# Performance work log

Hardware: AMD Instinct MI355X
Metric: run time of the kernel (lower is better)

The kernel has to match this reference:

```python
import jax, jax.numpy as jnp
import numpy as np
from jax import lax

DIM = 384
HEADS = 8
HEAD_DIM = DIM // HEADS
EPS = 1e-06


def setup_inputs() -> dict:
    key = jax.random.key(0)
    ks = jax.random.split(key, 16)
    B, N, C = 8, 4096, DIM
    s = 0.02
    inp = {
        "x": jax.random.normal(ks[0], (B, N, C), jnp.float32),
        "wq": jax.random.normal(ks[1], (C, C), jnp.float32) * s,
        "bq": jnp.zeros((C,), jnp.float32),
        "wk": jax.random.normal(ks[2], (C, C), jnp.float32) * s,
        "bk": jnp.zeros((C,), jnp.float32),
        "wv": jax.random.normal(ks[3], (C, C), jnp.float32) * s,
        "bv": jnp.zeros((C,), jnp.float32),
        "wg": jax.random.normal(ks[4], (C, C), jnp.float32) * s,
        "bg": jnp.zeros((C,), jnp.float32),
        "wo": jax.random.normal(ks[5], (C, C), jnp.float32) * s,
        "bo": jnp.zeros((C,), jnp.float32),
        "temperature": jnp.ones((HEADS, 1, 1), jnp.float32),
        "dw_w": jax.random.normal(ks[6], (C, 1, 3, 3), jnp.float32) * s,  # depthwise 3x3
        "dw_b": jnp.zeros((C,), jnp.float32),
        "pw_w": jax.random.normal(ks[7], (C, C), jnp.float32) * s,        # pointwise 1x1
        "pw_b": jnp.zeros((C,), jnp.float32),
    }
    return inp


def _phi(x):
    # exp(x - max) over last dim, numerically stable
    return jnp.exp(x - jnp.max(x, axis=-1, keepdims=True))


def _token_mixer(x, dw_w, dw_b, pw_w, pw_b):
    B, N, C = x.shape
    H = W = int(np.sqrt(N))
    feat = x.transpose(0, 2, 1).reshape(B, C, H, W)
    feat = lax.conv_general_dilated(
        feat, dw_w, window_strides=(1, 1), padding=((1, 1), (1, 1)),
        feature_group_count=C, dimension_numbers=("NCHW", "OIHW", "NCHW"))
    feat = feat + dw_b[None, :, None, None]
    feat = jnp.einsum("bchw,oc->bohw", feat, pw_w) + pw_b[None, :, None, None]
    return feat.reshape(B, C, N).transpose(0, 2, 1)


def reference(x, wq, bq, wk, bk, wv, bv, wg, bg, wo, bo, temperature,
              dw_w, dw_b, pw_w, pw_b):
    B, N, C = x.shape
    residual = x
    x = x + _token_mixer(x, dw_w, dw_b, pw_w, pw_b)

    def heads(y):  # [B,N,C] -> [B,H,N,d]
        return y.reshape(B, N, HEADS, HEAD_DIM).transpose(0, 2, 1, 3)

    q = heads(jnp.einsum("bnc,oc->bno", x, wq) + bq)
    k = heads(jnp.einsum("bnc,oc->bno", x, wk) + bk)
    v = heads(jnp.einsum("bnc,oc->bno", x, wv) + bv)
    g = heads(jnp.einsum("bnc,oc->bno", x, wg) + bg)

    q = _phi(q * temperature[None])       # temperature: [H,1,1] broadcasts over [B,H,N,d]
    k = _phi(k)
    v = v * jax.nn.sigmoid(g)

    kv = jnp.einsum("bhnd,bhne->bhde", k, v)     # [B,H,d,d]
    k_sum = jnp.sum(k, axis=2)                   # [B,H,d]
    num = jnp.einsum("bhnd,bhde->bhne", q, kv)   # [B,H,N,d]
    den = jnp.einsum("bhnd,bhd->bhn", q, k_sum)[..., None] + EPS
    out = num / den

    out = out.transpose(0, 2, 1, 3).reshape(B, N, C)
    out = jnp.einsum("bnc,oc->bno", out, wo) + bo
    return out + 0.0 * residual
```

## Files before the change

### kernel.cpp

```cpp
#include <hip/hip_runtime.h>
#include <math.h>

#define EPSF 1e-6f

typedef __attribute__((ext_vector_type(8))) short bf16x8;
typedef __attribute__((ext_vector_type(4))) float f32x4;
typedef unsigned short u16;
typedef unsigned int u32;

#define MFMA16(a,b,c) __builtin_amdgcn_mfma_f32_16x16x32_bf16((a),(b),(c),0,0,0)

__device__ __forceinline__ float bf2f(u16 u){
  union { u32 i; float f; } x; x.i = ((u32)u)<<16; return x.f;
}
__device__ __forceinline__ u16 f2bf(float f){
  u32 x = __builtin_bit_cast(u32, f);
  u32 r = (x + 0x7fffu + ((x >> 16) & 1u)) >> 16;
  return (u16)r;
}
__device__ __forceinline__ void gll16(const void* g, void* l){
  __builtin_amdgcn_global_load_lds(
      (const __attribute__((address_space(1))) u32*)g,
      (__attribute__((address_space(3))) u32*)l, 16, 0, 0);
}

__global__ __launch_bounds__(256) void k0_prep(
    const float* __restrict__ wq, const float* __restrict__ bq,
    const float* __restrict__ wk, const float* __restrict__ bk,
    const float* __restrict__ wv, const float* __restrict__ bv,
    const float* __restrict__ wg, const float* __restrict__ bg,
    const float* __restrict__ pw_w, const float* __restrict__ wo,
    u16* __restrict__ wpack, u16* __restrict__ pwb, u16* __restrict__ wob,
    float* __restrict__ bpack, float* __restrict__ kvacc, float* __restrict__ ksumacc)
{
  int idx = blockIdx.x*256 + threadIdx.x;
  const int NW = 1536*384;
  if (idx < NW) {
    int r = idx / 384, c = idx - r*384;
    int h = r / 192, s = (r % 192)/48, d = r % 48;
    const float* w = (s==0)?wq:(s==1)?wk:(s==2)?wv:wg;
    wpack[idx] = f2bf(w[(h*48+d)*384 + c]);
    if (c==0){
      const float* b = (s==0)?bq:(s==1)?bk:(s==2)?bv:bg;
      bpack[r] = b[h*48+d];
    }
  } else if (idx < NW + 147456) {
    pwb[idx - NW] = f2bf(pw_w[idx - NW]);
  } else if (idx < NW + 2*147456) {
    wob[idx - NW - 147456] = f2bf(wo[idx - NW - 147456]);
  } else if (idx < NW + 2*147456 + 147456) {
    kvacc[idx - NW - 2*147456] = 0.f;
  } else if (idx < NW + 2*147456 + 147456 + 3072) {
    ksumacc[idx - NW - 2*147456 - 147456] = 0.f;
  }
}

__global__ __launch_bounds__(256) void k1_dw(
    const float* __restrict__ x, const float* __restrict__ dw_w,
    const float* __restrict__ dw_b, u16* __restrict__ t)
{
  int idx = blockIdx.x*256 + threadIdx.x;
  int c4 = idx % 96; int rest = idx / 96;
  int jg = rest & 15; rest >>= 4;
  int i = rest & 63; int b = rest >> 6;
  int c0 = c4*4, j0 = jg*4;
  float wf[36];
  {
    const float4* wp = (const float4*)(dw_w + c0*9);
    #pragma unroll
    for (int k=0;k<9;k++){
      float4 v = wp[k];
      wf[4*k] = v.x; wf[4*k+1] = v.y; wf[4*k+2] = v.z; wf[4*k+3] = v.w;
    }
  }
  float4 bias = *(const float4*)(dw_b + c0);
  float acc[4][4];
  #pragma unroll
  for (int tk=0;tk<4;tk++){
    acc[tk][0]=bias.x; acc[tk][1]=bias.y; acc[tk][2]=bias.z; acc[tk][3]=bias.w;
  }
  const float* xb = x + ((size_t)b<<12)*384;
  #pragma unroll
  for (int di=-1; di<=1; ++di){
    int ii = i+di; if ((unsigned)ii >= 64u) continue;
    #pragma unroll
    for (int dj=-1; dj<=4; ++dj){
      int jj = j0+dj; if ((unsigned)jj >= 64u) continue;
      float4 xv = *(const float4*)(xb + (size_t)((ii<<6)+jj)*384 + c0);
      #pragma unroll
      for (int tk=0;tk<4;tk++){
        const int dd = dj - tk;
        if (dd < -1 || dd > 1) continue;
        const int tap = (di+1)*3 + (dd+1);
        acc[tk][0] = fmaf(xv.x, wf[0*9+tap], acc[tk][0]);
        acc[tk][1] = fmaf(xv.y, wf[1*9+tap], acc[tk][1]);
        acc[tk][2] = fmaf(xv.z, wf[2*9+tap], acc[tk][2]);
        acc[tk][3] = fmaf(xv.w, wf[3*9+tap], acc[tk][3]);
      }
    }
  }
  int mbase = (b<<12) + (i<<6) + j0;
  #pragma unroll
  for (int tk=0;tk<4;tk++){
    ushort4 o; o.x=f2bf(acc[tk][0]); o.y=f2bf(acc[tk][1]);
    o.z=f2bf(acc[tk][2]); o.w=f2bf(acc[tk][3]);
    *(ushort4*)(t + (size_t)(mbase+tk)*384 + c0) = o;
  }
}

__global__ __launch_bounds__(256) void k2_gemm_pw(
    const u16* __restrict__ t, const u16* __restrict__ pwb,
    const float* __restrict__ x, const float* __restrict__ pw_b,
    u16* __restrict__ xm)
{
  __shared__ __align__(16) u16 As[128*64];
  __shared__ __align__(16) u16 Bs[128*64];
  const int m0 = blockIdx.x * 128;
  const int n0 = blockIdx.y * 128;
  const int tid = threadIdx.x, w = tid>>6, l = tid&63;
  const f32x4 zf = {0.f,0.f,0.f,0.f};
  f32x4 acc[4][4];
  #pragma unroll
  for (int i=0;i<4;i++)
    #pragma unroll
    for (int j=0;j<4;j++) acc[i][j] = zf;

  for (int k0=0; k0<384; k0+=64) {
    #pragma unroll
    for (int i=0;i<4;i++){
      int ch = w*4+i;
      int row = ch*8 + (l>>3);
      gll16((const char*)t   + ((size_t)(m0+row)*384 + k0)*2 + (l&7)*16, (char*)As + ch*1024);
      gll16((const char*)pwb + ((size_t)(n0+row)*384 + k0)*2 + (l&7)*16, (char*)Bs + ch*1024);
    }
    __syncthreads();
    const int wr = (w>>1)*64, wc = (w&1)*64;
    #pragma unroll
    for (int kk=0; kk<64; kk+=32){
      bf16x8 a[4], bb[4];
      #pragma unroll
      for (int i=0;i<4;i++) a[i]  = *(const bf16x8*)&As[(wr + i*16 + (l&15))*64 + kk + (l>>4)*8];
      #pragma unroll
      for (int j=0;j<4;j++) bb[j] = *(const bf16x8*)&Bs[(wc + j*16 + (l&15))*64 + kk + (l>>4)*8];
      #pragma unroll
      for (int i=0;i<4;i++)
        #pragma unroll
        for (int j=0;j<4;j++)
          acc[i][j] = MFMA16(a[i], bb[j], acc[i][j]);
    }
    __syncthreads();
  }
  const int wr=(w>>1)*64, wc=(w&1)*64;
  #pragma unroll
  for (int j=0;j<4;j++){
    int n = n0 + wc + j*16 + (l&15);
    float bias = pw_b[n];
    #pragma unroll
    for (int i=0;i<4;i++)
      #pragma unroll
      for (int r=0;r<4;r++){
        int m = m0 + wr + i*16 + (l>>4)*4 + r;
        float v = acc[i][j][r] + x[(size_t)m*384 + n] + bias;
        xm[(size_t)m*384 + n] = f2bf(v);
      }
  }
}

__global__ __launch_bounds__(256) void k3_gemm_qkvg(
    const u16* __restrict__ xm, const u16* __restrict__ wpack,
    const float* __restrict__ bpack, const float* __restrict__ temperature,
    u16* __restrict__ qh, float* __restrict__ kvacc, float* __restrict__ ksumacc)
{
  __shared__ __align__(16) u16 smem[20480];
  u16* As = smem;
  u16* Bs = smem + 8192;
  const int m0 = blockIdx.x * 128;
  const int h  = blockIdx.y;
  const int tid = threadIdx.x, w = tid>>6, l = tid&63;
  const int lc = l & 15, hi = l >> 4;
  const f32x4 zf = {0.f,0.f,0.f,0.f};
  f32x4 acc[2][12];
  #pragma unroll
  for (int i=0;i<2;i++)
    #pragma unroll
    for (int j=0;j<12;j++) acc[i][j] = zf;

  for (int k0=0; k0<384; k0+=64){
    #pragma unroll
    for (int i=0;i<4;i++){
      int ch = w*4+i, row = ch*8 + (l>>3);
      gll16((const char*)xm + ((size_t)(m0+row)*384 + k0)*2 + (l&7)*16, (char*)As + ch*1024);
    }
    #pragma unroll
    for (int i=0;i<6;i++){
      int ch = w*6+i, row = ch*8 + (l>>3);
      gll16((const char*)wpack + ((size_t)(h*192+row)*384 + k0)*2 + (l&7)*16, (char*)Bs + ch*1024);
    }
    __syncthreads();
    const int rbase = w*32;
    #pragma unroll
    for (int kk=0; kk<64; kk+=32){
      bf16x8 a0 = *(const bf16x8*)&As[(rbase +      lc)*64 + kk + hi*8];
      bf16x8 a1 = *(const bf16x8*)&As[(rbase + 16 + lc)*64 + kk + hi*8];
      #pragma unroll
      for (int j=0;j<12;j++){
        bf16x8 bb = *(const bf16x8*)&Bs[(j*16 + lc)*64 + kk + hi*8];
        acc[0][j] = MFMA16(a0, bb, acc[0][j]);
        acc[1][j] = MFMA16(a1, bb, acc[1][j]);
      }
    }
    __syncthreads();
  }

  const float tq = temperature[h];
  const int b = m0 >> 12;
  const size_t bh = (size_t)b*8 + h;
  const int bb0 = h*192;
  float biasq[3], biask[3], biasv[3], biasg[3];
  #pragma unroll
  for (int j=0;j<3;j++){
    biasq[j] = bpack[bb0       + j*16 + lc];
    biask[j] = bpack[bb0 + 48  + j*16 + lc];
    biasv[j] = bpack[bb0 + 96  + j*16 + lc];
    biasg[j] = bpack[bb0 + 144 + j*16 + lc];
  }
  u16* kT = smem;
  u16* vT = smem + 6528;
  float ksp[3] = {0.f, 0.f, 0.f};

  #pragma unroll
  for (int i=0;i<2;i++){
    ushort4 kst[3], vst[3];
    #pragma unroll
    for (int r=0;r<4;r++){
      int m = m0 + w*32 + i*16 + hi*4 + r;
      int n = m & 4095;
      size_t rowq = (bh*4096 + n)*64;
      float q0=(acc[i][0][r]+biasq[0])*tq;
      float q1=(acc[i][1][r]+biasq[1])*tq;
      float q2=(acc[i][2][r]+biasq[2])*tq;
      float mx = fmaxf(q0,fmaxf(q1,q2));
      mx = fmaxf(mx, __shfl_xor(mx,1,64));
      mx = fmaxf(mx, __shfl_xor(mx,2,64));
      mx = fmaxf(mx, __shfl_xor(mx,4,64));
      mx = fmaxf(mx, __shfl_xor(mx,8,64));
      qh[rowq +      lc] = f2bf(expf(q0-mx));
      qh[rowq + 16 + lc] = f2bf(expf(q1-mx));
      qh[rowq + 32 + lc] = f2bf(expf(q2-mx));
      qh[rowq + 48 + lc] = 0;
      float s0=acc[i][3][r]+biask[0];
      float s1=acc[i][4][r]+biask[1];
      float s2=acc[i][5][r]+biask[2];
      float mk = fmaxf(s0,fmaxf(s1,s2));
      mk = fmaxf(mk, __shfl_xor(mk,1,64));
      mk = fmaxf(mk, __shfl_xor(mk,2,64));
      mk = fmaxf(mk, __shfl_xor(mk,4,64));
      mk = fmaxf(mk, __shfl_xor(mk,8,64));
      float k0e = expf(s0-mk), k1e = expf(s1-mk), k2e = expf(s2-mk);
      ksp[0] += k0e; ksp[1] += k1e; ksp[2] += k2e;
      u16 kq0=f2bf(k0e), kq1=f2bf(k1e), kq2=f2bf(k2e);
      u16 vq[3];
      #pragma unroll
      for (int j=0;j<3;j++){
        float vv = acc[i][6+j][r] + biasv[j];
        float gg = acc[i][9+j][r] + biasg[j];
        float sg = 1.f/(1.f + expf(-gg));
        vq[j] = f2bf(vv*sg);
      }
      if (r==0){ kst[0].x=kq0; kst[1].x=kq1; kst[2].x=kq2; vst[0].x=vq[0]; vst[1].x=vq[1]; vst[2].x=vq[2]; }
      if (r==1){ kst[0].y=kq0; kst[1].y=kq1; kst[2].y=kq2; vst[0].y=vq[0]; vst[1].y=vq[1]; vst[2].y=vq[2]; }
      if (r==2){ kst[0].z=kq0; kst[1].z=kq1; kst[2].z=kq2; vst[0].z=vq[0]; vst[1].z=vq[1]; vst[2].z=vq[2]; }
      if (r==3){ kst[0].w=kq0; kst[1].w=kq1; kst[2].w=kq2; vst[0].w=vq[0]; vst[1].w=vq[1]; vst[2].w=vq[2]; }
    }
    int mb = w*32 + i*16 + hi*4;
    #pragma unroll
    for (int j=0;j<3;j++){
      *(ushort4*)&kT[(j*16+lc)*136 + mb] = kst[j];
      *(ushort4*)&vT[(j*16+lc)*136 + mb] = vst[j];
    }
  }
  __syncthreads();

  bf16x8 af[3], bfv[3];
  #pragma unroll
  for (int da=0;da<3;da++) af[da]  = *(const bf16x8*)&kT[(da*16+lc)*136 + w*32 + hi*8];
  #pragma unroll
  for (int eb=0;eb<3;eb++) bfv[eb] = *(const bf16x8*)&vT[(eb*16+lc)*136 + w*32 + hi*8];
  f32x4 a2[3][3];
  #pragma unroll
  for (int da=0;da<3;da++)
    #pragma unroll
    for (int eb=0;eb<3;eb++)
      a2[da][eb] = MFMA16(af[da], bfv[eb], zf);
  __syncthreads();
  float* pb = (float*)smem + w*2304;
  #pragma unroll
  for (int da=0;da<3;da++)
    #pragma unroll
    for (int eb=0;eb<3;eb++)
      #pragma unroll
      for (int rr=0;rr<4;rr++)
        pb[(da*16 + hi*4 + rr)*48 + eb*16 + lc] = a2[da][eb][rr];
  __syncthreads();
  float* p0 = (float*)smem;
  for (int u=tid; u<2304; u+=256){
    float s = p0[u] + p0[2304+u] + p0[4608+u] + p0[6912+u];
    atomicAdd(kvacc + bh*2304 + u, s);
  }
  #pragma unroll
  for (int j=0;j<3;j++){
    ksp[j] += __shfl_xor(ksp[j],16,64);
    ksp[j] += __shfl_xor(ksp[j],32,64);
  }
  if (hi==0){
    atomicAdd(ksumacc + bh*48 +      lc, ksp[0]);
    atomicAdd(ksumacc + bh*48 + 16 + lc, ksp[1]);
    atomicAdd(ksumacc + bh*48 + 32 + lc, ksp[2]);
  }
}

__global__ __launch_bounds__(256) void k5_red(
    const float* __restrict__ kvacc, const float* __restrict__ ksumacc,
    u16* __restrict__ kvp)
{
  int bh = blockIdx.x, tid = threadIdx.x;
  for (int u=tid; u<4096; u+=256){
    int e = u >> 6, d = u & 63;
    float v = 0.f;
    if (e < 48 && d < 48)       v = kvacc[(size_t)bh*2304 + d*48 + e];
    else if (e == 48 && d < 48) v = ksumacc[bh*48 + d];
    kvp[((size_t)bh*64 + e)*64 + d] = f2bf(v);
  }
}

__global__ __launch_bounds__(256) void k6_num(
    const u16* __restrict__ qh, const u16* __restrict__ kvp, u16* __restrict__ ah)
{
  __shared__ __align__(16) u16 As[256*64];
  __shared__ __align__(16) u16 Bs[64*64];
  const int bh = blockIdx.x >> 4, nc = blockIdx.x & 15;
  const int tid = threadIdx.x, w = tid>>6, l = tid&63;
  const f32x4 zf = {0.f,0.f,0.f,0.f};
  const uint4* ga = (const uint4*)(qh + ((size_t)bh*4096 + nc*256)*64);
  #pragma unroll
  for (int it=0; it<8; ++it) ((uint4*)As)[it*256+tid] = ga[it*256+tid];
  const uint4* gb = (const uint4*)(kvp + (size_t)bh*4096);
  #pragma unroll
  for (int it=0; it<2; ++it) ((uint4*)Bs)[it*256+tid] = gb[it*256+tid];
  __syncthreads();
  f32x4 acc[4][4];
  #pragma unroll
  for (int i=0;i<4;i++)
    #pragma unroll
    for (int j=0;j<4;j++) acc[i][j] = zf;
  const int rbase = w*64;
  #pragma unroll
  for (int kk=0; kk<64; kk+=32){
    bf16x8 a[4], bb[4];
    #pragma unroll
    for (int i=0;i<4;i++) a[i]  = *(const bf16x8*)&As[(rbase + i*16 + (l&15))*64 + kk + (l>>4)*8];
    #pragma unroll
    for (int j=0;j<4;j++) bb[j] = *(const bf16x8*)&Bs[(j*16 + (l&15))*64 + kk + (l>>4)*8];
    #pragma unroll
    for (int i=0;i<4;i++)
      #pragma unroll
      for (int j=0;j<4;j++)
        acc[i][j] = MFMA16(a[i], bb[j], acc[i][j]);
  }
  const int b = bh >> 3, h = bh & 7;
  #pragma unroll
  for (int i=0;i<4;i++){
    #pragma unroll
    for (int r=0;r<4;r++){
      float den = __shfl(acc[i][3][r], l & 48, 64) + EPSF;
      float rd = 1.f/den;
      int n = nc*256 + rbase + i*16 + (l>>4)*4 + r;
      size_t ob = ((size_t)b*4096 + n)*384 + h*48;
      ah[ob +      (l&15)] = f2bf(acc[i][0][r]*rd);
      ah[ob + 16 + (l&15)] = f2bf(acc[i][1][r]*rd);
      ah[ob + 32 + (l&15)] = f2bf(acc[i][2][r]*rd);
    }
  }
}

__global__ __launch_bounds__(256) void k7_gemm_out(
    const u16* __restrict__ ah, const u16* __restrict__ wob,
    const float* __restrict__ bo, float* __restrict__ out)
{
  __shared__ __align__(16) u16 As[128*64];
  __shared__ __align__(16) u16 Bs[128*64];
  const int m0 = blockIdx.x * 128;
  const int n0 = blockIdx.y * 128;
  const int tid = threadIdx.x, w = tid>>6, l = tid&63;
  const f32x4 zf = {0.f,0.f,0.f,0.f};
  f32x4 acc[4][4];
  #pragma unroll
  for (int i=0;i<4;i++)
    #pragma unroll
    for (int j=0;j<4;j++) acc[i][j] = zf;

  for (int k0=0; k0<384; k0+=64) {
    #pragma unroll
    for (int i=0;i<4;i++){
      int ch = w*4+i;
      int row = ch*8 + (l>>3);
      gll16((const char*)ah  + ((size_t)(m0+row)*384 + k0)*2 + (l&7)*16, (char*)As + ch*1024);
      gll16((const char*)wob + ((size_t)(n0+row)*384 + k0)*2 + (l&7)*16, (char*)Bs + ch*1024);
    }
    __syncthreads();
    const int wr = (w>>1)*64, wc = (w&1)*64;
    #pragma unroll
    for (int kk=0; kk<64; kk+=32){
      bf16x8 a[4], bb[4];
      #pragma unroll
      for (int i=0;i<4;i++) a[i]  = *(const bf16x8*)&As[(wr + i*16 + (l&15))*64 + kk + (l>>4)*8];
      #pragma unroll
      for (int j=0;j<4;j++) bb[j] = *(const bf16x8*)&Bs[(wc + j*16 + (l&15))*64 + kk + (l>>4)*8];
      #pragma unroll
      for (int i=0;i<4;i++)
        #pragma unroll
        for (int j=0;j<4;j++)
          acc[i][j] = MFMA16(a[i], bb[j], acc[i][j]);
    }
    __syncthreads();
  }
  const int wr=(w>>1)*64, wc=(w&1)*64;
  #pragma unroll
  for (int j=0;j<4;j++){
    int n = n0 + wc + j*16 + (l&15);
    float bias = bo[n];
    #pragma unroll
    for (int i=0;i<4;i++)
      #pragma unroll
      for (int r=0;r<4;r++){
        int m = m0 + wr + i*16 + (l>>4)*4 + r;
        out[(size_t)m*384 + n] = acc[i][j][r] + bias;
      }
  }
}

extern "C" void kernel_launch(void* const* d_in, const int* in_sizes, int n_in,
                              void* d_out, int out_size, void* d_ws, size_t ws_size,
                              hipStream_t stream)
{
  const float* x    = (const float*)d_in[0];
  const float* wq   = (const float*)d_in[1];
  const float* bq   = (const float*)d_in[2];
  const float* wk   = (const float*)d_in[3];
  const float* bk   = (const float*)d_in[4];
  const float* wv   = (const float*)d_in[5];
  const float* bv   = (const float*)d_in[6];
  const float* wg   = (const float*)d_in[7];
  const float* bg   = (const float*)d_in[8];
  const float* wo   = (const float*)d_in[9];
  const float* bo   = (const float*)d_in[10];
  const float* temp = (const float*)d_in[11];
  const float* dw_w = (const float*)d_in[12];
  const float* dw_b = (const float*)d_in[13];
  const float* pw_w = (const float*)d_in[14];
  const float* pw_b = (const float*)d_in[15];
  float* out = (float*)d_out;
  char* ws = (char*)d_ws;

  u16*   t       = (u16*)(ws + 0);
  u16*   xm      = (u16*)(ws + 25165824);
  u16*   qh      = (u16*)(ws + 50331648);
  u16*   wpack   = (u16*)(ws + 83886080);
  u16*   pwb     = (u16*)(ws + 85065728);
  u16*   wob     = (u16*)(ws + 85360640);
  float* bpack   = (float*)(ws + 85655552);
  float* kvacc   = (float*)(ws + 85661696);
  float* ksumacc = (float*)(ws + 86251520);
  u16*   kvp     = (u16*)(ws + 86263808);

  k0_prep<<<4044, 256, 0, stream>>>(wq,bq,wk,bk,wv,bv,wg,bg,pw_w,wo,
                                    wpack,pwb,wob,bpack,kvacc,ksumacc);
  k1_dw<<<3072, 256, 0, stream>>>(x, dw_w, dw_b, t);
  k2_gemm_pw<<<dim3(256,3), 256, 0, stream>>>(t, pwb, x, pw_b, xm);
  k3_gemm_qkvg<<<dim3(256,8), 256, 0, stream>>>(xm, wpack, bpack, temp, qh, kvacc, ksumacc);
  k5_red<<<64, 256, 0, stream>>>(kvacc, ksumacc, kvp);
  k6_num<<<1024, 256, 0, stream>>>(qh, kvp, t );
  k7_gemm_out<<<dim3(256,3), 256, 0, stream>>>(t, wob, bo, out);
}
```

Before: 207.2 us.

## Use k-chunk-major LDS layout to avoid bank conflicts and compact q storage

Reorganizes the shared-memory tiles in all GEMM kernels from row-major (64 bf16 per row) to a chunk-major layout where each 8-element k-chunk is contiguous across rows. This is meant to remove LDS bank conflicts on the 16-byte MFMA operand reads. The exp(q) tile is now staged in LDS and written to global memory in a matching chunked layout with 48 instead of 64 columns, which drops the zero padding from the q buffer and cuts its global traffic. The kv buffer layout is changed to match, and the consumer kernel zero-fills the padding chunks in LDS itself. The cost is more complex indexing, an extra LDS staging pass in k3, and a global load pattern where each lane now fetches a different row per 16-byte load.

```diff
diff --git a/kernel.cpp b/kernel.cpp
--- a/kernel.cpp
+++ b/kernel.cpp
@@ -118,6 +118,7 @@
   const int m0 = blockIdx.x * 128;
   const int n0 = blockIdx.y * 128;
   const int tid = threadIdx.x, w = tid>>6, l = tid&63;
+  const int lc = l & 15, hi = l >> 4;
   const f32x4 zf = {0.f,0.f,0.f,0.f};
   f32x4 acc[4][4];
   #pragma unroll
@@ -127,21 +128,22 @@
 
   for (int k0=0; k0<384; k0+=64) {
     #pragma unroll
-    for (int i=0;i<4;i++){
-      int ch = w*4+i;
-      int row = ch*8 + (l>>3);
-      gll16((const char*)t   + ((size_t)(m0+row)*384 + k0)*2 + (l&7)*16, (char*)As + ch*1024);
-      gll16((const char*)pwb + ((size_t)(n0+row)*384 + k0)*2 + (l&7)*16, (char*)Bs + ch*1024);
+    for (int c=0;c<4;c++){
+      int chunk = 2*c + (w>>1);
+      int row = (w&1)*64 + l;
+      gll16((const char*)t   + ((size_t)(m0+row)*384 + k0 + chunk*8)*2, (char*)As + (c*256+w*64)*16);
+      gll16((const char*)pwb + ((size_t)(n0+row)*384 + k0 + chunk*8)*2, (char*)Bs + (c*256+w*64)*16);
     }
     __syncthreads();
     const int wr = (w>>1)*64, wc = (w&1)*64;
     #pragma unroll
     for (int kk=0; kk<64; kk+=32){
+      const int ca = (kk>>3) + hi;
       bf16x8 a[4], bb[4];
       #pragma unroll
-      for (int i=0;i<4;i++) a[i]  = *(const bf16x8*)&As[(wr + i*16 + (l&15))*64 + kk + (l>>4)*8];
-      #pragma unroll
-      for (int j=0;j<4;j++) bb[j] = *(const bf16x8*)&Bs[(wc + j*16 + (l&15))*64 + kk + (l>>4)*8];
+      for (int i=0;i<4;i++) a[i]  = *(const bf16x8*)&As[(ca*128 + wr + i*16 + lc)*8];
+      #pragma unroll
+      for (int j=0;j<4;j++) bb[j] = *(const bf16x8*)&Bs[(ca*128 + wc + j*16 + lc)*8];
       #pragma unroll
       for (int i=0;i<4;i++)
         #pragma unroll
@@ -153,13 +155,13 @@
   const int wr=(w>>1)*64, wc=(w&1)*64;
   #pragma unroll
   for (int j=0;j<4;j++){
-    int n = n0 + wc + j*16 + (l&15);
+    int n = n0 + wc + j*16 + lc;
     float bias = pw_b[n];
     #pragma unroll
     for (int i=0;i<4;i++)
       #pragma unroll
       for (int r=0;r<4;r++){
-        int m = m0 + wr + i*16 + (l>>4)*4 + r;
+        int m = m0 + wr + i*16 + hi*4 + r;
         float v = acc[i][j][r] + x[(size_t)m*384 + n] + bias;
         xm[(size_t)m*384 + n] = f2bf(v);
       }
@@ -187,24 +189,28 @@
 
   for (int k0=0; k0<384; k0+=64){
     #pragma unroll
-    for (int i=0;i<4;i++){
-      int ch = w*4+i, row = ch*8 + (l>>3);
-      gll16((const char*)xm + ((size_t)(m0+row)*384 + k0)*2 + (l&7)*16, (char*)As + ch*1024);
-    }
-    #pragma unroll
-    for (int i=0;i<6;i++){
-      int ch = w*6+i, row = ch*8 + (l>>3);
-      gll16((const char*)wpack + ((size_t)(h*192+row)*384 + k0)*2 + (l&7)*16, (char*)Bs + ch*1024);
+    for (int c=0;c<4;c++){
+      int chunk = 2*c + (w>>1);
+      int row = (w&1)*64 + l;
+      gll16((const char*)xm + ((size_t)(m0+row)*384 + k0 + chunk*8)*2, (char*)As + (c*256+w*64)*16);
+    }
+    #pragma unroll
+    for (int c=0;c<6;c++){
+      int q = c*4 + w;
+      int chunk = q/3;
+      int row = (q - chunk*3)*64 + l;
+      gll16((const char*)wpack + ((size_t)(h*192+row)*384 + k0 + chunk*8)*2, (char*)Bs + q*1024);
     }
     __syncthreads();
     const int rbase = w*32;
     #pragma unroll
     for (int kk=0; kk<64; kk+=32){
-      bf16x8 a0 = *(const bf16x8*)&As[(rbase +      lc)*64 + kk + hi*8];
-      bf16x8 a1 = *(const bf16x8*)&As[(rbase + 16 + lc)*64 + kk + hi*8];
+      const int ca = (kk>>3) + hi;
+      bf16x8 a0 = *(const bf16x8*)&As[(ca*128 + rbase +      lc)*8];
+      bf16x8 a1 = *(const bf16x8*)&As[(ca*128 + rbase + 16 + lc)*8];
       #pragma unroll
       for (int j=0;j<12;j++){
-        bf16x8 bb = *(const bf16x8*)&Bs[(j*16 + lc)*64 + kk + hi*8];
+        bf16x8 bb = *(const bf16x8*)&Bs[(ca*192 + j*16 + lc)*8];
         acc[0][j] = MFMA16(a0, bb, acc[0][j]);
         acc[1][j] = MFMA16(a1, bb, acc[1][j]);
       }
@@ -224,8 +230,9 @@
     biasv[j] = bpack[bb0 + 96  + j*16 + lc];
     biasg[j] = bpack[bb0 + 144 + j*16 + lc];
   }
-  u16* kT = smem;
-  u16* vT = smem + 6528;
+  u16* kT  = smem;
+  u16* vT  = smem + 6528;
+  u16* qls = smem + 13056;
   float ksp[3] = {0.f, 0.f, 0.f};
 
   #pragma unroll
@@ -233,9 +240,7 @@
     ushort4 kst[3], vst[3];
     #pragma unroll
     for (int r=0;r<4;r++){
-      int m = m0 + w*32 + i*16 + hi*4 + r;
-      int n = m & 4095;
-      size_t rowq = (bh*4096 + n)*64;
+      int row = w*32 + i*16 + hi*4 + r;
       float q0=(acc[i][0][r]+biasq[0])*tq;
       float q1=(acc[i][1][r]+biasq[1])*tq;
       float q2=(acc[i][2][r]+biasq[2])*tq;
@@ -244,10 +249,10 @@
       mx = fmaxf(mx, __shfl_xor(mx,2,64));
       mx = fmaxf(mx, __shfl_xor(mx,4,64));
       mx = fmaxf(mx, __shfl_xor(mx,8,64));
-      qh[rowq +      lc] = f2bf(expf(q0-mx));
-      qh[rowq + 16 + lc] = f2bf(expf(q1-mx));
-      qh[rowq + 32 + lc] = f2bf(expf(q2-mx));
-      qh[rowq + 48 + lc] = 0;
+      int ro8 = row*8 + (lc&7);
+      qls[((lc>>3)  )*1024 + ro8] = f2bf(expf(q0-mx));
+      qls[((lc>>3)+2)*1024 + ro8] = f2bf(expf(q1-mx));
+      qls[((lc>>3)+4)*1024 + ro8] = f2bf(expf(q2-mx));
       float s0=acc[i][3][r]+biask[0];
       float s1=acc[i][4][r]+biask[1];
       float s2=acc[i][5][r]+biask[2];
@@ -281,6 +286,18 @@
   }
   __syncthreads();
 
+  {
+    const int tile = (m0 & 4095) >> 8;
+    const int half = (m0 >> 7) & 1;
+    size_t gqb = ((size_t)bh*4096 + tile*256)*48;
+    #pragma unroll
+    for (int it=0; it<3; ++it){
+      int s = it*256 + tid;
+      int g = (s>>7)*256 + half*128 + (s&127);
+      *(uint4*)(qh + gqb + (size_t)g*8) = *(const uint4*)&qls[s*8];
+    }
+  }
+
   bf16x8 af[3], bfv[3];
   #pragma unroll
   for (int da=0;da<3;da++) af[da]  = *(const bf16x8*)&kT[(da*16+lc)*136 + w*32 + hi*8];
@@ -329,7 +346,7 @@
     float v = 0.f;
     if (e < 48 && d < 48)       v = kvacc[(size_t)bh*2304 + d*48 + e];
     else if (e == 48 && d < 48) v = ksumacc[bh*48 + d];
-    kvp[((size_t)bh*64 + e)*64 + d] = f2bf(v);
+    kvp[(size_t)bh*4096 + (d>>3)*512 + e*8 + (d&7)] = f2bf(v);
   }
 }
 
@@ -340,10 +357,14 @@
   __shared__ __align__(16) u16 Bs[64*64];
   const int bh = blockIdx.x >> 4, nc = blockIdx.x & 15;
   const int tid = threadIdx.x, w = tid>>6, l = tid&63;
+  const int lc = l & 15, hi = l >> 4;
   const f32x4 zf = {0.f,0.f,0.f,0.f};
-  const uint4* ga = (const uint4*)(qh + ((size_t)bh*4096 + nc*256)*64);
-  #pragma unroll
-  for (int it=0; it<8; ++it) ((uint4*)As)[it*256+tid] = ga[it*256+tid];
+  const uint4* ga = (const uint4*)(qh + ((size_t)bh*4096 + nc*256)*48);
+  #pragma unroll
+  for (int it=0; it<6; ++it) ((uint4*)As)[it*256+tid] = ga[it*256+tid];
+  uint4 z4 = {0,0,0,0};
+  *(uint4*)&As[(1536+tid)*8] = z4;
+  *(uint4*)&As[(1792+tid)*8] = z4;
   const uint4* gb = (const uint4*)(kvp + (size_t)bh*4096);
   #pragma unroll
   for (int it=0; it<2; ++it) ((uint4*)Bs)[it*256+tid] = gb[it*256+tid];
@@ -356,11 +377,12 @@
   const int rbase = w*64;
   #pragma unroll
   for (int kk=0; kk<64; kk+=32){
+    const int ca = (kk>>3) + hi;
     bf16x8 a[4], bb[4];
     #pragma unroll
-    for (int i=0;i<4;i++) a[i]  = *(const bf16x8*)&As[(rbase + i*16 + (l&15))*64 + kk + (l>>4)*8];
-    #pragma unroll
-    for (int j=0;j<4;j++) bb[j] = *(const bf16x8*)&Bs[(j*16 + (l&15))*64 + kk + (l>>4)*8];
+    for (int i=0;i<4;i++) a[i]  = *(const bf16x8*)&As[(ca*256 + rbase + i*16 + lc)*8];
+    #pragma unroll
+    for (int j=0;j<4;j++) bb[j] = *(const bf16x8*)&Bs[(ca*64 + j*16 + lc)*8];
     #pragma unroll
     for (int i=0;i<4;i++)
       #pragma unroll
@@ -374,11 +396,11 @@
     for (int r=0;r<4;r++){
       float den = __shfl(acc[i][3][r], l & 48, 64) + EPSF;
       float rd = 1.f/den;
-      int n = nc*256 + rbase + i*16 + (l>>4)*4 + r;
+      int n = nc*256 + rbase + i*16 + hi*4 + r;
       size_t ob = ((size_t)b*4096 + n)*384 + h*48;
-      ah[ob +      (l&15)] = f2bf(acc[i][0][r]*rd);
-      ah[ob + 16 + (l&15)] = f2bf(acc[i][1][r]*rd);
-      ah[ob + 32 + (l&15)] = f2bf(acc[i][2][r]*rd);
+      ah[ob +      lc] = f2bf(acc[i][0][r]*rd);
+      ah[ob + 16 + lc] = f2bf(acc[i][1][r]*rd);
+      ah[ob + 32 + lc] = f2bf(acc[i][2][r]*rd);
     }
   }
 }
@@ -392,6 +414,7 @@
   const int m0 = blockIdx.x * 128;
   const int n0 = blockIdx.y * 128;
   const int tid = threadIdx.x, w = tid>>6, l = tid&63;
+  const int lc = l & 15, hi = l >> 4;
   const f32x4 zf = {0.f,0.f,0.f,0.f};
   f32x4 acc[4][4];
   #pragma unroll
@@ -401,21 +424,22 @@
 
   for (int k0=0; k0<384; k0+=64) {
     #pragma unroll
-    for (int i=0;i<4;i++){
-      int ch = w*4+i;
-      int row = ch*8 + (l>>3);
-      gll16((const char*)ah  + ((size_t)(m0+row)*384 + k0)*2 + (l&7)*16, (char*)As + ch*1024);
-      gll16((const char*)wob + ((size_t)(n0+row)*384 + k0)*2 + (l&7)*16, (char*)Bs + ch*1024);
+    for (int c=0;c<4;c++){
+      int chunk = 2*c + (w>>1);
+      int row = (w&1)*64 + l;
+      gll16((const char*)ah  + ((size_t)(m0+row)*384 + k0 + chunk*8)*2, (char*)As + (c*256+w*64)*16);
+      gll16((const char*)wob + ((size_t)(n0+row)*384 + k0 + chunk*8)*2, (char*)Bs + (c*256+w*64)*16);
     }
     __syncthreads();
     const int wr = (w>>1)*64, wc = (w&1)*64;
     #pragma unroll
     for (int kk=0; kk<64; kk+=32){
+      const int ca = (kk>>3) + hi;
       bf16x8 a[4], bb[4];
       #pragma unroll
-      for (int i=0;i<4;i++) a[i]  = *(const bf16x8*)&As[(wr + i*16 + (l&15))*64 + kk + (l>>4)*8];
-      #pragma unroll
-      for (int j=0;j<4;j++) bb[j] = *(const bf16x8*)&Bs[(wc + j*16 + (l&15))*64 + kk + (l>>4)*8];
+      for (int i=0;i<4;i++) a[i]  = *(const bf16x8*)&As[(ca*128 + wr + i*16 + lc)*8];
+      #pragma unroll
+      for (int j=0;j<4;j++) bb[j] = *(const bf16x8*)&Bs[(ca*128 + wc + j*16 + lc)*8];
       #pragma unroll
       for (int i=0;i<4;i++)
         #pragma unroll
@@ -427,13 +451,13 @@
   const int wr=(w>>1)*64, wc=(w&1)*64;
   #pragma unroll
   for (int j=0;j<4;j++){
-    int n = n0 + wc + j*16 + (l&15);
+    int n = n0 + wc + j*16 + lc;
     float bias = bo[n];
     #pragma unroll
     for (int i=0;i<4;i++)
       #pragma unroll
       for (int r=0;r<4;r++){
-        int m = m0 + wr + i*16 + (l>>4)*4 + r;
+        int m = m0 + wr + i*16 + hi*4 + r;
         out[(size_t)m*384 + n] = acc[i][j][r] + bias;
       }
   }
```

Result: slower. 230.4 us (+11.2%).

## Restructure QKVG GEMM into 1024-thread blocks with double-buffered swizzled LDS

Applied to the files above, without the earlier changes.

The QKVG projection kernel now uses 1024-thread blocks, each covering 256 rows. The K loop uses double-buffered LDS stages with XOR-swizzled chunk placement, so the next global-to-LDS load is issued while the current tile feeds the MFMAs, and one barrier per K step is removed. Exponentiated q rows are staged in LDS and written out as coalesced 16-byte stores, replacing scattered 2-byte stores. The kv partials are reduced across 8 waves, which halves the number of global atomics. The risks are that the 112 KB LDS footprint limits the CU to one block, and that the (1024,4) launch bound may force a tight register budget and cause spills.

```diff
diff --git a/kernel.cpp b/kernel.cpp
--- a/kernel.cpp
+++ b/kernel.cpp
@@ -10,9 +10,6 @@
 
 #define MFMA16(a,b,c) __builtin_amdgcn_mfma_f32_16x16x32_bf16((a),(b),(c),0,0,0)
 
-__device__ __forceinline__ float bf2f(u16 u){
-  union { u32 i; float f; } x; x.i = ((u32)u)<<16; return x.f;
-}
 __device__ __forceinline__ u16 f2bf(float f){
   u32 x = __builtin_bit_cast(u32, f);
   u32 r = (x + 0x7fffu + ((x >> 16) & 1u)) >> 16;
@@ -166,50 +163,67 @@
   }
 }
 
-__global__ __launch_bounds__(256) void k3_gemm_qkvg(
+__global__ __launch_bounds__(1024, 4) void k3_gemm_qkvg(
     const u16* __restrict__ xm, const u16* __restrict__ wpack,
     const float* __restrict__ bpack, const float* __restrict__ temperature,
     u16* __restrict__ qh, float* __restrict__ kvacc, float* __restrict__ ksumacc)
 {
-  __shared__ __align__(16) u16 smem[20480];
-  u16* As = smem;
-  u16* Bs = smem + 8192;
-  const int m0 = blockIdx.x * 128;
+  __shared__ __align__(16) u16 smem[57344];
+  const int m0 = blockIdx.x * 256;
   const int h  = blockIdx.y;
   const int tid = threadIdx.x, w = tid>>6, l = tid&63;
   const int lc = l & 15, hi = l >> 4;
   const f32x4 zf = {0.f,0.f,0.f,0.f};
-  f32x4 acc[2][12];
-  #pragma unroll
-  for (int i=0;i<2;i++)
-    #pragma unroll
-    for (int j=0;j<12;j++) acc[i][j] = zf;
-
-  for (int k0=0; k0<384; k0+=64){
-    #pragma unroll
-    for (int i=0;i<4;i++){
-      int ch = w*4+i, row = ch*8 + (l>>3);
-      gll16((const char*)xm + ((size_t)(m0+row)*384 + k0)*2 + (l&7)*16, (char*)As + ch*1024);
-    }
-    #pragma unroll
-    for (int i=0;i<6;i++){
-      int ch = w*6+i, row = ch*8 + (l>>3);
-      gll16((const char*)wpack + ((size_t)(h*192+row)*384 + k0)*2 + (l&7)*16, (char*)Bs + ch*1024);
+  f32x4 acc[12];
+  #pragma unroll
+  for (int j=0;j<12;j++) acc[j] = zf;
+
+  #define K3_STAGE(T, CUR) do {                                               \
+    const int k0_ = (T)*64;                                                   \
+    u16* Ab_ = smem + (CUR)*16384;                                            \
+    u16* Bb_ = smem + 32768 + (CUR)*12288;                                    \
+    _Pragma("unroll")                                                         \
+    for (int c=0;c<2;c++){                                                    \
+      int ci = c*1024 + tid;                                                  \
+      int R = ci>>3, osw = (ci&7) ^ (R&7);                                    \
+      gll16((const char*)xm + ((size_t)(m0+R)*384 + k0_)*2 + osw*16,          \
+            (char*)Ab_ + (c*1024 + w*64)*16);                                 \
+    }                                                                         \
+    {                                                                         \
+      int ci = tid;                                                           \
+      int R = ci>>3, osw = (ci&7) ^ (R&7);                                    \
+      gll16((const char*)wpack + ((size_t)(h*192+R)*384 + k0_)*2 + osw*16,    \
+            (char*)Bb_ + (w*64)*16);                                          \
+    }                                                                         \
+    if (tid < 512){                                                           \
+      int ci = 1024 + tid;                                                    \
+      int R = ci>>3, osw = (ci&7) ^ (R&7);                                    \
+      gll16((const char*)wpack + ((size_t)(h*192+R)*384 + k0_)*2 + osw*16,    \
+            (char*)Bb_ + (1024 + w*64)*16);                                   \
+    }                                                                         \
+  } while(0)
+
+  K3_STAGE(0, 0);
+  __syncthreads();
+  int cur = 0;
+  const int rbase = w*16;
+  for (int t=0; t<6; ++t){
+    if (t < 5) K3_STAGE(t+1, cur^1);
+    const u16* Ab = smem + cur*16384;
+    const u16* Bb = smem + 32768 + cur*12288;
+    #pragma unroll
+    for (int kk=0; kk<64; kk+=32){
+      const int ca = (kk>>3) + hi;
+      const int sw = ca ^ (lc&7);
+      bf16x8 a0 = *(const bf16x8*)&Ab[((rbase+lc)*8 + sw)*8];
+      #pragma unroll
+      for (int j=0;j<12;j++){
+        bf16x8 bb = *(const bf16x8*)&Bb[((j*16+lc)*8 + sw)*8];
+        acc[j] = MFMA16(a0, bb, acc[j]);
+      }
     }
     __syncthreads();
-    const int rbase = w*32;
-    #pragma unroll
-    for (int kk=0; kk<64; kk+=32){
-      bf16x8 a0 = *(const bf16x8*)&As[(rbase +      lc)*64 + kk + hi*8];
-      bf16x8 a1 = *(const bf16x8*)&As[(rbase + 16 + lc)*64 + kk + hi*8];
-      #pragma unroll
-      for (int j=0;j<12;j++){
-        bf16x8 bb = *(const bf16x8*)&Bs[(j*16 + lc)*64 + kk + hi*8];
-        acc[0][j] = MFMA16(a0, bb, acc[0][j]);
-        acc[1][j] = MFMA16(a1, bb, acc[1][j]);
-      }
-    }
-    __syncthreads();
+    cur ^= 1;
   }
 
   const float tq = temperature[h];
@@ -224,33 +238,31 @@
     biasv[j] = bpack[bb0 + 96  + j*16 + lc];
     biasg[j] = bpack[bb0 + 144 + j*16 + lc];
   }
-  u16* kT = smem;
-  u16* vT = smem + 6528;
+  u16* qls = smem;
+  u16* vT  = smem + 12288;
+  u16* kT  = smem + 32768;
   float ksp[3] = {0.f, 0.f, 0.f};
 
-  #pragma unroll
-  for (int i=0;i<2;i++){
+  {
     ushort4 kst[3], vst[3];
     #pragma unroll
     for (int r=0;r<4;r++){
-      int m = m0 + w*32 + i*16 + hi*4 + r;
-      int n = m & 4095;
-      size_t rowq = (bh*4096 + n)*64;
-      float q0=(acc[i][0][r]+biasq[0])*tq;
-      float q1=(acc[i][1][r]+biasq[1])*tq;
-      float q2=(acc[i][2][r]+biasq[2])*tq;
+      int row = w*16 + hi*4 + r;
+      float q0=(acc[0][r]+biasq[0])*tq;
+      float q1=(acc[1][r]+biasq[1])*tq;
+      float q2=(acc[2][r]+biasq[2])*tq;
       float mx = fmaxf(q0,fmaxf(q1,q2));
       mx = fmaxf(mx, __shfl_xor(mx,1,64));
       mx = fmaxf(mx, __shfl_xor(mx,2,64));
       mx = fmaxf(mx, __shfl_xor(mx,4,64));
       mx = fmaxf(mx, __shfl_xor(mx,8,64));
-      qh[rowq +      lc] = f2bf(expf(q0-mx));
-      qh[rowq + 16 + lc] = f2bf(expf(q1-mx));
-      qh[rowq + 32 + lc] = f2bf(expf(q2-mx));
-      qh[rowq + 48 + lc] = 0;
-      float s0=acc[i][3][r]+biask[0];
-      float s1=acc[i][4][r]+biask[1];
-      float s2=acc[i][5][r]+biask[2];
+      int p8 = row*8 + (lc&7);
+      qls[(lc>>3)*2048     + p8] = f2bf(expf(q0-mx));
+      qls[((lc>>3)+2)*2048 + p8] = f2bf(expf(q1-mx));
+      qls[((lc>>3)+4)*2048 + p8] = f2bf(expf(q2-mx));
+      float s0=acc[3][r]+biask[0];
+      float s1=acc[4][r]+biask[1];
+      float s2=acc[5][r]+biask[2];
       float mk = fmaxf(s0,fmaxf(s1,s2));
       mk = fmaxf(mk, __shfl_xor(mk,1,64));
       mk = fmaxf(mk, __shfl_xor(mk,2,64));
@@ -262,8 +274,8 @@
       u16 vq[3];
       #pragma unroll
       for (int j=0;j<3;j++){
-        float vv = acc[i][6+j][r] + biasv[j];
-        float gg = acc[i][9+j][r] + biasg[j];
+        float vv = acc[6+j][r] + biasv[j];
+        float gg = acc[9+j][r] + biasg[j];
         float sg = 1.f/(1.f + expf(-gg));
         vq[j] = f2bf(vv*sg);
       }
@@ -272,40 +284,61 @@
       if (r==2){ kst[0].z=kq0; kst[1].z=kq1; kst[2].z=kq2; vst[0].z=vq[0]; vst[1].z=vq[1]; vst[2].z=vq[2]; }
       if (r==3){ kst[0].w=kq0; kst[1].w=kq1; kst[2].w=kq2; vst[0].w=vq[0]; vst[1].w=vq[1]; vst[2].w=vq[2]; }
     }
-    int mb = w*32 + i*16 + hi*4;
+    int mb = w*16 + hi*4;
     #pragma unroll
     for (int j=0;j<3;j++){
-      *(ushort4*)&kT[(j*16+lc)*136 + mb] = kst[j];
-      *(ushort4*)&vT[(j*16+lc)*136 + mb] = vst[j];
+      *(ushort4*)&kT[(j*16+lc)*264 + mb] = kst[j];
+      *(ushort4*)&vT[(j*16+lc)*264 + mb] = vst[j];
     }
   }
   __syncthreads();
 
-  bf16x8 af[3], bfv[3];
-  #pragma unroll
-  for (int da=0;da<3;da++) af[da]  = *(const bf16x8*)&kT[(da*16+lc)*136 + w*32 + hi*8];
-  #pragma unroll
-  for (int eb=0;eb<3;eb++) bfv[eb] = *(const bf16x8*)&vT[(eb*16+lc)*136 + w*32 + hi*8];
+  {
+    size_t gqb = ((size_t)bh*4096 + (m0 & 4095))*64;
+    #pragma unroll
+    for (int it=0; it<2; ++it){
+      int idx = it*1024 + tid;
+      int row = idx>>3, ch = idx&7;
+      uint4 v = {0,0,0,0};
+      if (ch < 6) v = *(const uint4*)&qls[ch*2048 + row*8];
+      *(uint4*)(qh + gqb + (size_t)row*64 + ch*8) = v;
+    }
+  }
+
   f32x4 a2[3][3];
-  #pragma unroll
-  for (int da=0;da<3;da++)
-    #pragma unroll
-    for (int eb=0;eb<3;eb++)
-      a2[da][eb] = MFMA16(af[da], bfv[eb], zf);
+  if (w < 8){
+    bf16x8 af[3], bfv[3];
+    #pragma unroll
+    for (int da=0;da<3;da++) af[da]  = *(const bf16x8*)&kT[(da*16+lc)*264 + w*32 + hi*8];
+    #pragma unroll
+    for (int eb=0;eb<3;eb++) bfv[eb] = *(const bf16x8*)&vT[(eb*16+lc)*264 + w*32 + hi*8];
+    #pragma unroll
+    for (int da=0;da<3;da++)
+      #pragma unroll
+      for (int eb=0;eb<3;eb++)
+        a2[da][eb] = MFMA16(af[da], bfv[eb], zf);
+  }
   __syncthreads();
-  float* pb = (float*)smem + w*2304;
-  #pragma unroll
-  for (int da=0;da<3;da++)
-    #pragma unroll
-    for (int eb=0;eb<3;eb++)
-      #pragma unroll
-      for (int rr=0;rr<4;rr++)
-        pb[(da*16 + hi*4 + rr)*48 + eb*16 + lc] = a2[da][eb][rr];
+  if (w < 8){
+    float* pb = (w<4) ? ((float*)smem + w*2304)
+                      : ((float*)(smem + 32768) + (w-4)*2304);
+    #pragma unroll
+    for (int da=0;da<3;da++)
+      #pragma unroll
+      for (int eb=0;eb<3;eb++)
+        #pragma unroll
+        for (int rr=0;rr<4;rr++)
+          pb[(da*16 + hi*4 + rr)*48 + eb*16 + lc] = a2[da][eb][rr];
+  }
   __syncthreads();
-  float* p0 = (float*)smem;
-  for (int u=tid; u<2304; u+=256){
-    float s = p0[u] + p0[2304+u] + p0[4608+u] + p0[6912+u];
-    atomicAdd(kvacc + bh*2304 + u, s);
+  {
+    float* pA = (float*)smem;
+    float* pB = (float*)(smem + 32768);
+    for (int u=tid; u<2304; u+=1024){
+      float s = pA[u] + pA[2304+u] + pA[4608+u] + pA[6912+u]
+              + pB[u] + pB[2304+u] + pB[4608+u] + pB[6912+u];
+      atomicAdd(kvacc + bh*2304 + u, s);
+    }
   }
   #pragma unroll
   for (int j=0;j<3;j++){
@@ -317,6 +350,7 @@
     atomicAdd(ksumacc + bh*48 + 16 + lc, ksp[1]);
     atomicAdd(ksumacc + bh*48 + 32 + lc, ksp[2]);
   }
+  #undef K3_STAGE
 }
 
 __global__ __launch_bounds__(256) void k5_red(
@@ -477,7 +511,7 @@
                                     wpack,pwb,wob,bpack,kvacc,ksumacc);
   k1_dw<<<3072, 256, 0, stream>>>(x, dw_w, dw_b, t);
   k2_gemm_pw<<<dim3(256,3), 256, 0, stream>>>(t, pwb, x, pw_b, xm);
-  k3_gemm_qkvg<<<dim3(256,8), 256, 0, stream>>>(xm, wpack, bpack, temp, qh, kvacc, ksumacc);
+  k3_gemm_qkvg<<<dim3(128,8), 1024, 0, stream>>>(xm, wpack, bpack, temp, qh, kvacc, ksumacc);
   k5_red<<<64, 256, 0, stream>>>(kvacc, ksumacc, kvp);
   k6_num<<<1024, 256, 0, stream>>>(qh, kvp, t );
   k7_gemm_out<<<dim3(256,3), 256, 0, stream>>>(t, wob, bo, out);
```

Result: slower. 223.4 us (+7.8%).
